# Performance work log

Hardware: AMD Instinct MI355X
Metric: run time of the kernel (lower is better)

Reference implementation:

```python
import jax, jax.numpy as jnp
import numpy as np

W_FLOAT = 13.7
W_CEIL = 14                      # int(ceil(w))
RGB_IDX = (3, 7, 10)             # round(w/4), round(w/2), round(3w/4)


def setup_inputs() -> dict:
    key = jax.random.key(0)
    B, H, W = 1, 2048, 3072
    x = jax.random.uniform(key, (B, 1, H, W), jnp.float32)
    # lenticule-start mask: one start every w_ceil columns (periodic), so every
    # spreader window of width w_ceil contains exactly one start (z_norm >= 1)
    z = (jnp.arange(W) % W_CEIL == 0).astype(jnp.float32)
    z = jnp.broadcast_to(z[None, None, None, :], (B, 1, H, W)).copy()
    return {"x": x, "z": z}


def _moving_sum(a, win):
    cs = jnp.cumsum(a, axis=-1)
    shifted = jnp.concatenate([jnp.zeros_like(cs[..., :win]), cs[..., :-win]], axis=-1)
    return cs - shifted


def _forward(x, z):
    B, _, H, W = x.shape
    # --- Space2Features: the eye/delay one-hot convs are a pure shift-gather:
    # x_exp[b,i,h,p] = x[b,0,h,p+i] * z[b,0,h,p]
    xp = jnp.pad(x, ((0, 0), (0, 0), (0, 0), (0, W_CEIL - 1)))
    idx = jnp.arange(W)[None, :] + jnp.arange(W_CEIL)[:, None]        # [w_ceil, W]
    x_shift = jnp.moveaxis(jnp.take(xp, idx, axis=3)[:, 0], 2, 1)     # [B, w_ceil, H, W]
    x_exp = x_shift * z                                               # gate by mask
    # --- RGBExtractor_fixed (autotune off): RGB is one-hot over the channel
    # dim, so the 1x1 conv is channel selection at the fixed R/G/B offsets
    x_rgb = x_exp[:, jnp.array(RGB_IDX)]                              # [B, 3, H, W]
    # rgb_filter_image[b,c,h,p] = z[b,0,h,p - idx_c]  (right-shift of mask)
    zp = jnp.pad(z, ((0, 0), (0, 0), (0, 0), (W_CEIL - 1, 0)))
    ridx = jnp.arange(W)[None, :] - jnp.array(RGB_IDX)[:, None] + (W_CEIL - 1)  # [3, W]
    rgb_filter_image = jnp.moveaxis(jnp.take(zp, ridx, axis=3)[:, 0], 2, 1)     # [B,3,H,W]
    # --- LenticuleSpreader: per-channel backward moving sum of width w_ceil,
    # then normalize by the spread mask
    y = _moving_sum(x_rgb, W_CEIL) / _moving_sum(z, W_CEIL)
    return y, rgb_filter_image


def reference(x, z):
    return _forward(x, z)
```

## Files before the change

### kernel.cpp

```cpp
#include <hip/hip_runtime.h>

constexpr int Wd  = 3072;
constexpr int WC  = 14;
constexpr int XL  = 12;
constexpr int XR  = 16;
constexpr int ZL  = 16;

__global__ __launch_bounds__(256)
void color_restore_kernel(const float* __restrict__ xg,
                          const float* __restrict__ zg,
                          float* __restrict__ out, int Hn)
{
    __shared__ __align__(16) float xs[XL + Wd + XR];
    __shared__ __align__(16) float zs[ZL + Wd];

    const int h = blockIdx.x;
    const int t = threadIdx.x;

    const float4* xrow = (const float4*)(xg + (size_t)h * Wd);
    const float4* zrow = (const float4*)(zg + (size_t)h * Wd);
    float4* xs4 = (float4*)(xs + XL);
    float4* zs4 = (float4*)(zs + ZL);
#pragma unroll
    for (int i = 0; i < 3; ++i) {
        const int idx = t + i * 256;
        xs4[idx] = xrow[idx];
        zs4[idx] = zrow[idx];
    }
    if (t < XL) xs[t] = 0.f;
    if (t < XR) xs[XL + Wd + t] = 0.f;
    if (t < ZL) zs[t] = 0.f;
    __syncthreads();

    const int plane = Hn * Wd;
    float* yout = out;
    float* rout = out + 3 * (size_t)plane;

#pragma unroll
    for (int p = 0; p < 3; ++p) {
        const int w0 = p * 1024 + 4 * t;

        float zbuf[20];
        {
            float4* zb = (float4*)zbuf;
            const int zblk = (ZL + w0 - 13) >> 2;
#pragma unroll
            for (int i = 0; i < 5; ++i) zb[i] = ((const float4*)zs)[zblk + i];
        }
        float xbuf[28];
        {
            float4* xb = (float4*)xbuf;
            const int xblk = (XL + w0 - 10) >> 2;
#pragma unroll
            for (int i = 0; i < 7; ++i) xb[i] = ((const float4*)xs)[xblk + i];
        }

        float den = 0.f, n0 = 0.f, n1 = 0.f, n2 = 0.f;
#pragma unroll
        for (int s = 0; s < WC; ++s) {
            const float zj = zbuf[3 + s];
            den += zj;
            n0 = fmaf(xbuf[s + 2], zj, n0);
            n1 = fmaf(xbuf[s + 6], zj, n1);
            n2 = fmaf(xbuf[s + 9], zj, n2);
        }

        float y0[4], y1[4], y2[4], r0[4], r1[4], r2[4];
#pragma unroll
        for (int q = 0; q < 4; ++q) {
            if (q > 0) {
                const float zin  = zbuf[16 + q];
                const float zot  = zbuf[2 + q];
                den += zin - zot;
                n0 += xbuf[15 + q] * zin - xbuf[1 + q] * zot;
                n1 += xbuf[19 + q] * zin - xbuf[5 + q] * zot;
                n2 += xbuf[22 + q] * zin - xbuf[8 + q] * zot;
            }
            const float rinv = __builtin_amdgcn_rcpf(den);
            y0[q] = n0 * rinv;
            y1[q] = n1 * rinv;
            y2[q] = n2 * rinv;
            r0[q] = zbuf[13 + q];
            r1[q] = zbuf[9 + q];
            r2[q] = zbuf[6 + q];
        }

        const int off = h * Wd + w0;
        *(float4*)(yout + off)             = make_float4(y0[0], y0[1], y0[2], y0[3]);
        *(float4*)(yout + plane + off)     = make_float4(y1[0], y1[1], y1[2], y1[3]);
        *(float4*)(yout + 2 * plane + off) = make_float4(y2[0], y2[1], y2[2], y2[3]);
        *(float4*)(rout + off)             = make_float4(r0[0], r0[1], r0[2], r0[3]);
        *(float4*)(rout + plane + off)     = make_float4(r1[0], r1[1], r1[2], r1[3]);
        *(float4*)(rout + 2 * plane + off) = make_float4(r2[0], r2[1], r2[2], r2[3]);
    }
}

extern "C" void kernel_launch(void* const* d_in, const int* in_sizes, int n_in,
                              void* d_out, int out_size, void* d_ws, size_t ws_size,
                              hipStream_t stream)
{
    const float* x = (const float*)d_in[0];
    const float* z = (const float*)d_in[1];
    float* out = (float*)d_out;
    const int Hn = in_sizes[0] / Wd;
    color_restore_kernel<<<dim3(Hn), dim3(256), 0, stream>>>(x, z, out, Hn);
}
```

Before: 188.5 us.

## Drop LDS staging, load halos directly from global, split rows across blocks

Removes the shared-memory row staging and __syncthreads. Each thread now loads its overlapping x/z windows straight from global memory as vector loads, with a scalar bounds-checked path at the row edges. The grid is split into three segments per row for more blocks, and outputs use nontemporal stores. Neighbouring threads re-read overlapping halos, so the kernel relies on cache hits to absorb the redundant global traffic.

```diff
diff --git a/kernel.cpp b/kernel.cpp
--- a/kernel.cpp
+++ b/kernel.cpp
@@ -1,98 +1,102 @@
 #include <hip/hip_runtime.h>
 
-constexpr int Wd  = 3072;
-constexpr int WC  = 14;
-constexpr int XL  = 12;
-constexpr int XR  = 16;
-constexpr int ZL  = 16;
+constexpr int Wd = 3072;
+constexpr int WC = 14;
 
-__global__ __launch_bounds__(256)
+typedef float fvec4 __attribute__((ext_vector_type(4)));
+
+__global__ __launch_bounds__(256, 2)
 void color_restore_kernel(const float* __restrict__ xg,
                           const float* __restrict__ zg,
                           float* __restrict__ out, int Hn)
 {
-    __shared__ __align__(16) float xs[XL + Wd + XR];
-    __shared__ __align__(16) float zs[ZL + Wd];
+    const int h   = blockIdx.y;
+    const int seg = blockIdx.x;
+    const int t   = threadIdx.x;
+    const int w0  = seg * 1024 + 4 * t;
 
-    const int h = blockIdx.x;
-    const int t = threadIdx.x;
+    const float* __restrict__ xrow = xg + (size_t)h * Wd;
+    const float* __restrict__ zrow = zg + (size_t)h * Wd;
 
-    const float4* xrow = (const float4*)(xg + (size_t)h * Wd);
-    const float4* zrow = (const float4*)(zg + (size_t)h * Wd);
-    float4* xs4 = (float4*)(xs + XL);
-    float4* zs4 = (float4*)(zs + ZL);
+    float xb[28];
+    float zb[20];
+
+    if (w0 >= 16 && w0 <= Wd - 16) {
+        const fvec4* xp4 = (const fvec4*)(xrow + (w0 - 12));
+        const fvec4* zp4 = (const fvec4*)(zrow + (w0 - 16));
+        fvec4 xq[7], zq[5];
 #pragma unroll
-    for (int i = 0; i < 3; ++i) {
-        const int idx = t + i * 256;
-        xs4[idx] = xrow[idx];
-        zs4[idx] = zrow[idx];
+        for (int i = 0; i < 7; ++i) xq[i] = xp4[i];
+#pragma unroll
+        for (int i = 0; i < 5; ++i) zq[i] = zp4[i];
+#pragma unroll
+        for (int i = 0; i < 7; ++i) {
+            xb[4 * i + 0] = xq[i].x; xb[4 * i + 1] = xq[i].y;
+            xb[4 * i + 2] = xq[i].z; xb[4 * i + 3] = xq[i].w;
+        }
+#pragma unroll
+        for (int i = 0; i < 5; ++i) {
+            zb[4 * i + 0] = zq[i].x; zb[4 * i + 1] = zq[i].y;
+            zb[4 * i + 2] = zq[i].z; zb[4 * i + 3] = zq[i].w;
+        }
+    } else {
+#pragma unroll
+        for (int i = 0; i < 28; ++i) {
+            const int k = w0 - 12 + i;
+            xb[i] = (k >= 0 && k < Wd) ? xrow[k] : 0.f;
+        }
+#pragma unroll
+        for (int i = 0; i < 20; ++i) {
+            const int k = w0 - 16 + i;
+            zb[i] = (k >= 0 && k < Wd) ? zrow[k] : 0.f;
+        }
     }
-    if (t < XL) xs[t] = 0.f;
-    if (t < XR) xs[XL + Wd + t] = 0.f;
-    if (t < ZL) zs[t] = 0.f;
-    __syncthreads();
+
+    float den = 0.f, n0 = 0.f, n1 = 0.f, n2 = 0.f;
+#pragma unroll
+    for (int s = 0; s < WC; ++s) {
+        const float zj = zb[3 + s];
+        den += zj;
+        n0 = fmaf(xb[s + 2], zj, n0);
+        n1 = fmaf(xb[s + 6], zj, n1);
+        n2 = fmaf(xb[s + 9], zj, n2);
+    }
+
+    float y0[4], y1[4], y2[4];
+#pragma unroll
+    for (int q = 0; q < 4; ++q) {
+        if (q > 0) {
+            const float zin = zb[16 + q];
+            const float zot = zb[2 + q];
+            den += zin - zot;
+            n0 += xb[15 + q] * zin - xb[1 + q] * zot;
+            n1 += xb[19 + q] * zin - xb[5 + q] * zot;
+            n2 += xb[22 + q] * zin - xb[8 + q] * zot;
+        }
+        const float rinv = __builtin_amdgcn_rcpf(den);
+        y0[q] = n0 * rinv;
+        y1[q] = n1 * rinv;
+        y2[q] = n2 * rinv;
+    }
 
     const int plane = Hn * Wd;
+    const int off   = h * Wd + w0;
     float* yout = out;
     float* rout = out + 3 * (size_t)plane;
 
-#pragma unroll
-    for (int p = 0; p < 3; ++p) {
-        const int w0 = p * 1024 + 4 * t;
-
-        float zbuf[20];
-        {
-            float4* zb = (float4*)zbuf;
-            const int zblk = (ZL + w0 - 13) >> 2;
-#pragma unroll
-            for (int i = 0; i < 5; ++i) zb[i] = ((const float4*)zs)[zblk + i];
-        }
-        float xbuf[28];
-        {
-            float4* xb = (float4*)xbuf;
-            const int xblk = (XL + w0 - 10) >> 2;
-#pragma unroll
-            for (int i = 0; i < 7; ++i) xb[i] = ((const float4*)xs)[xblk + i];
-        }
-
-        float den = 0.f, n0 = 0.f, n1 = 0.f, n2 = 0.f;
-#pragma unroll
-        for (int s = 0; s < WC; ++s) {
-            const float zj = zbuf[3 + s];
-            den += zj;
-            n0 = fmaf(xbuf[s + 2], zj, n0);
-            n1 = fmaf(xbuf[s + 6], zj, n1);
-            n2 = fmaf(xbuf[s + 9], zj, n2);
-        }
-
-        float y0[4], y1[4], y2[4], r0[4], r1[4], r2[4];
-#pragma unroll
-        for (int q = 0; q < 4; ++q) {
-            if (q > 0) {
-                const float zin  = zbuf[16 + q];
-                const float zot  = zbuf[2 + q];
-                den += zin - zot;
-                n0 += xbuf[15 + q] * zin - xbuf[1 + q] * zot;
-                n1 += xbuf[19 + q] * zin - xbuf[5 + q] * zot;
-                n2 += xbuf[22 + q] * zin - xbuf[8 + q] * zot;
-            }
-            const float rinv = __builtin_amdgcn_rcpf(den);
-            y0[q] = n0 * rinv;
-            y1[q] = n1 * rinv;
-            y2[q] = n2 * rinv;
-            r0[q] = zbuf[13 + q];
-            r1[q] = zbuf[9 + q];
-            r2[q] = zbuf[6 + q];
-        }
-
-        const int off = h * Wd + w0;
-        *(float4*)(yout + off)             = make_float4(y0[0], y0[1], y0[2], y0[3]);
-        *(float4*)(yout + plane + off)     = make_float4(y1[0], y1[1], y1[2], y1[3]);
-        *(float4*)(yout + 2 * plane + off) = make_float4(y2[0], y2[1], y2[2], y2[3]);
-        *(float4*)(rout + off)             = make_float4(r0[0], r0[1], r0[2], r0[3]);
-        *(float4*)(rout + plane + off)     = make_float4(r1[0], r1[1], r1[2], r1[3]);
-        *(float4*)(rout + 2 * plane + off) = make_float4(r2[0], r2[1], r2[2], r2[3]);
-    }
+    fvec4 v;
+    v.x = y0[0]; v.y = y0[1]; v.z = y0[2]; v.w = y0[3];
+    __builtin_nontemporal_store(v, (fvec4*)(yout + off));
+    v.x = y1[0]; v.y = y1[1]; v.z = y1[2]; v.w = y1[3];
+    __builtin_nontemporal_store(v, (fvec4*)(yout + plane + off));
+    v.x = y2[0]; v.y = y2[1]; v.z = y2[2]; v.w = y2[3];
+    __builtin_nontemporal_store(v, (fvec4*)(yout + 2 * plane + off));
+    v.x = zb[13]; v.y = zb[14]; v.z = zb[15]; v.w = zb[16];
+    __builtin_nontemporal_store(v, (fvec4*)(rout + off));
+    v.x = zb[9]; v.y = zb[10]; v.z = zb[11]; v.w = zb[12];
+    __builtin_nontemporal_store(v, (fvec4*)(rout + plane + off));
+    v.x = zb[6]; v.y = zb[7]; v.z = zb[8]; v.w = zb[9];
+    __builtin_nontemporal_store(v, (fvec4*)(rout + 2 * plane + off));
 }
 
 extern "C" void kernel_launch(void* const* d_in, const int* in_sizes, int n_in,
@@ -103,5 +107,5 @@
     const float* z = (const float*)d_in[1];
     float* out = (float*)d_out;
     const int Hn = in_sizes[0] / Wd;
-    color_restore_kernel<<<dim3(Hn), dim3(256), 0, stream>>>(x, z, out, Hn);
+    color_restore_kernel<<<dim3(3, Hn), dim3(256), 0, stream>>>(x, z, out, Hn);
 }
```

Measured after the change: 195.5 us. 1.04x slower.
